# Performance work log

Measured on AMD Instinct MI355X. Metric: run time of the kernel, lower is better.

The kernel has to match this reference:

```python
import jax, jax.numpy as jnp
import numpy as np

TRAN_DIM = 768
N_HEADS = 8
HEAD_DIM = 96
INNER = N_HEADS * HEAD_DIM  # 768


def setup_inputs() -> dict:
    key = jax.random.key(0)
    k1, k2, k3, k4, k5 = jax.random.split(key, 5)
    x = jax.random.normal(k1, (16, 1024, TRAN_DIM), dtype=jnp.float32)
    s_in = 1.0 / np.sqrt(TRAN_DIM)
    W_qkv = jax.random.uniform(k2, (TRAN_DIM, INNER * 3), jnp.float32, -s_in, s_in)
    b_qkv = jax.random.uniform(k3, (INNER * 3,), jnp.float32, -s_in, s_in)
    s_o = 1.0 / np.sqrt(INNER)
    W_out = jax.random.uniform(k4, (INNER, TRAN_DIM), jnp.float32, -s_o, s_o)
    b_out = jax.random.uniform(k5, (TRAN_DIM,), jnp.float32, -s_o, s_o)
    return {"x": x, "W_qkv": W_qkv, "b_qkv": b_qkv, "W_out": W_out, "b_out": b_out}


def reference(x, W_qkv, b_qkv, W_out, b_out):
    B, N, _ = x.shape
    qkv = x @ W_qkv + b_qkv  # [B, N, 3*INNER]
    q, k, v = jnp.split(qkv, 3, axis=-1)
    # [B, N, INNER] -> [B, H, N, D]
    def to_heads(t):
        return t.reshape(B, N, N_HEADS, HEAD_DIM).transpose(0, 2, 1, 3)
    q, k, v = to_heads(q), to_heads(k), to_heads(v)
    scale = HEAD_DIM ** (-0.5)
    dots = jnp.einsum('bhnd,bhmd->bhnm', q, k) * scale
    attn = jax.nn.softmax(dots, axis=-1)
    out = jnp.einsum('bhnm,bhmd->bhnd', attn, v)
    out = out.transpose(0, 2, 1, 3).reshape(B, N, INNER)
    return out @ W_out + b_out
```

## Files before the change

kernel.cpp:

```cpp
#include <hip/hip_runtime.h>
#include <hip/hip_bf16.h>


#define DEVINL __device__ __forceinline__

typedef __attribute__((ext_vector_type(8))) short s16x8;
typedef __attribute__((ext_vector_type(4))) short s16x4;
typedef __attribute__((ext_vector_type(4))) float f32x4;
typedef __attribute__((ext_vector_type(16))) float f32x16;

DEVINL short f2bf(float f) {
  union { float f; unsigned u; } c; c.f = f;
  unsigned r = c.u + 0x7FFFu + ((c.u >> 16) & 1u);
  return (short)(r >> 16);
}
DEVINL float asf(unsigned u) {
  union { unsigned u; float f; } c; c.u = u; return c.f;
}
DEVINL unsigned pack2(float a, float b) {
  union { float f; unsigned u; } ca, cb; ca.f = a; cb.f = b;
  return (ca.u >> 16) | (cb.u & 0xffff0000u);
}
DEVINL int swap23(int k) { return (k & ~12) | ((k & 4) << 1) | ((k & 8) >> 1); }

DEVINL void gload_lds16(const short* g, short* lds) {
  __builtin_amdgcn_global_load_lds((const __attribute__((address_space(1))) void*)g,
                                   (__attribute__((address_space(3))) void*)lds, 16, 0, 0);
}


__global__ void cvt_x_kernel(const float* __restrict__ in, short* __restrict__ out) {
  int i = blockIdx.x * 256 + threadIdx.x;
  float4 v = ((const float4*)in)[i];
  s16x4 o = { f2bf(v.x), f2bf(v.y), f2bf(v.z), f2bf(v.w) };
  *(s16x4*)(out + (size_t)i * 4) = o;
}

__global__ void tcvt_kernel(const float* __restrict__ in, short* __restrict__ out, int R, int C) {
  __shared__ float t[32][33];
  int tx = threadIdx.x & 31, ty = threadIdx.x >> 5;
  int r0 = blockIdx.y * 32, c0 = blockIdx.x * 32;
#pragma unroll
  for (int i = 0; i < 4; i++) {
    int r = ty + i * 8;
    t[r][tx] = in[(size_t)(r0 + r) * C + c0 + tx];
  }
  __syncthreads();
#pragma unroll
  for (int i = 0; i < 4; i++) {
    int r = ty + i * 8;
    out[(size_t)(c0 + r) * R + r0 + tx] = f2bf(t[tx][r]);
  }
}

__global__ void vtrans_kernel(const short* __restrict__ qkvb, short* __restrict__ out) {
  __shared__ short t[32][34];
  int tx = threadIdx.x & 31, ty = threadIdx.x >> 5;
  int d0 = blockIdx.x * 32, n0 = blockIdx.y * 32;
  int pair = blockIdx.z;
  int b = pair >> 3, h = pair & 7;
#pragma unroll
  for (int i = 0; i < 4; i++) {
    int r = ty + i * 8;
    t[r][tx] = qkvb[(size_t)(b * 1024 + n0 + r) * 2304 + 1536 + h * 96 + d0 + tx];
  }
  __syncthreads();
  size_t obase = (size_t)pair * 96 * 1024;
#pragma unroll
  for (int i = 0; i < 4; i++) {
    int r = ty + i * 8;
    out[obase + (size_t)(d0 + r) * 1024 + n0 + tx] = t[tx][r];
  }
}


template <int MODE>
__global__ __launch_bounds__(512, 4) void gemm2(const short* __restrict__ A, const short* __restrict__ Bt,
                                                const float* __restrict__ bias, int K, int nTn,
                                                short* __restrict__ qkvb, float* __restrict__ outf) {
  __shared__ short lds[36864];
  short* const ldsA = lds;
  short* const ldsB = lds + 24576;
  const int tid = threadIdx.x;
  const int l = tid & 63, w = tid >> 6;
  const int lo = l & 15, hi = l >> 4;
  const int wm = w >> 1, wn = w & 1;

  int cpx = gridDim.x >> 3;
  int bid = blockIdx.x;
  int swz = (bid & 7) * cpx + (bid >> 3);
  int tm = swz / nTn, tn = swz - tm * nTn;

  const int NKT = K >> 5;

  const int Ls = tid >> 3, s7 = tid & 7;
  const int pS = (s7 >> 2) & 1;
  const int cS = (s7 & 3) ^ (Ls & 3);
  const int rho = 2 * Ls + pS;
  const int gA = ((rho >> 5) << 6) + (rho & 31);
  const short* aS0 = A + (size_t)(tm * 256 + gA) * K + cS * 8;
  const short* aS1 = aS0 + (size_t)32 * K;
  const short* bS = Bt + (size_t)(tn * 128 + rho) * K + cS * 8;

#define ST_A(j, q, bs) gload_lds16(((q) ? aS1 : aS0) + (j) * 32, ldsA + ((bs) * 2 + (q)) * 4096 + tid * 8)
#define ST_B(j, bs)    gload_lds16(bS + (j) * 32, ldsB + (bs) * 4096 + tid * 8)

  const int LaBase = wm * 16 + (lo >> 1);
  const int LbBase = wn * 32 + (lo >> 1);
  const int pp = (lo & 1) << 2;

  f32x4 acc[4][4] = {};

#define RD_A(AF, bc, qm) do {                                                    \
    const short* base_ = ldsA + ((bc) * 2 + (qm)) * 4096;                        \
    _Pragma("unroll") for (int mi = 0; mi < 2; mi++) {                           \
      int La_ = LaBase + mi * 8;                                                 \
      AF[mi] = *(const s16x8*)(base_ + La_ * 64 + (((hi ^ (La_ & 3)) + pp) << 3)); } } while (0)
#define RD_B(BF, bc) do {                                                        \
    const short* base_ = ldsB + (bc) * 4096;                                     \
    _Pragma("unroll") for (int b = 0; b < 4; b++) {                              \
      int Lb_ = LbBase + b * 8;                                                  \
      BF[b] = *(const s16x8*)(base_ + Lb_ * 64 + (((hi ^ (Lb_ & 3)) + pp) << 3)); } } while (0)

#define MM8(a0, AF, BF) do {                                                     \
    __builtin_amdgcn_s_setprio(1);                                               \
    _Pragma("unroll") for (int mi = 0; mi < 2; mi++)                             \
      _Pragma("unroll") for (int b = 0; b < 4; b++)                              \
        acc[(a0) + mi][b] = __builtin_amdgcn_mfma_f32_16x16x32_bf16(             \
            AF[mi], BF[b], acc[(a0) + mi][b], 0, 0, 0);                          \
    __builtin_amdgcn_s_setprio(0); } while (0)

#define WAITV(n) asm volatile("s_waitcnt vmcnt(" #n ")" ::: "memory")
#define BARR() do { __builtin_amdgcn_sched_barrier(0); __builtin_amdgcn_s_barrier(); \
                    __builtin_amdgcn_sched_barrier(0); } while (0)

  ST_A(0, 0, 0); ST_B(0, 0); ST_A(0, 1, 0);
  ST_A(1, 0, 1); ST_B(1, 1); ST_A(1, 1, 1);
  WAITV(3);
  __builtin_amdgcn_s_barrier();

  s16x8 af[2], bf[4];
  int bc = 0;
#pragma unroll 1
  for (int kt = 0; kt < NKT; kt++) {
    int bs = (bc == 0) ? 2 : bc - 1;
    RD_A(af, bc, 0);
    RD_B(bf, bc);
    if (kt + 2 < NKT) { ST_A(kt + 2, 0, bs); ST_B(kt + 2, bs); }
    MM8(0, af, bf);
    RD_A(af, bc, 1);
    if (kt + 2 < NKT) ST_A(kt + 2, 1, bs);
    MM8(2, af, bf);
    if (kt + 2 < NKT) {
      WAITV(3);
    } else if (kt + 2 == NKT) {
      WAITV(0);
    }
    BARR();
    bc = (bc == 2) ? 0 : bc + 1;
  }
#undef ST_A
#undef ST_B
#undef RD_A
#undef RD_B
#undef MM8
#undef WAITV
#undef BARR

  if (MODE == 0) {
    const float qscale = 0.14724444757204526f;
    __syncthreads();
#pragma unroll
    for (int b = 0; b < 4; b++) {
      int colr = wn * 64 + b * 16 + lo;
      int coln = tn * 128 + colr;
      float bv = bias[coln];
      float scl = (coln < 768) ? qscale : 1.0f;
#pragma unroll
      for (int a = 0; a < 4; a++)
#pragma unroll
        for (int j = 0; j < 4; j++) {
          int rowr = wm * 64 + a * 16 + hi * 4 + j;
          lds[rowr * 128 + colr] = f2bf((acc[a][b][j] + bv) * scl);
        }
    }
    __syncthreads();
    short* dstb = qkvb + (size_t)(tm * 256) * 2304 + tn * 128;
#pragma unroll
    for (int k = 0; k < 8; k++) {
      int g = k * 512 + tid;
      int r = g >> 4, c = g & 15;
      *(s16x8*)(dstb + (size_t)r * 2304 + c * 8) = *(const s16x8*)(lds + r * 128 + c * 8);
    }
  } else {
#pragma unroll
    for (int b = 0; b < 4; b++) {
      int coln = tn * 128 + wn * 64 + b * 16 + lo;
      float bv = bias[coln];
#pragma unroll
      for (int a = 0; a < 4; a++)
#pragma unroll
        for (int j = 0; j < 4; j++) {
          int rowm = tm * 256 + wm * 64 + a * 16 + hi * 4 + j;
          outf[(size_t)rowm * 768 + coln] = acc[a][b][j] + bv;
        }
    }
  }
}


__global__ __launch_bounds__(256) void attn_kernel(const short* __restrict__ qkvb,
                                                   const short* __restrict__ vtb,
                                                   short* __restrict__ attn_out) {
  __shared__ short Klds[64 * 104];
  __shared__ short Vlds[96 * 64];
  int tid = threadIdx.x, lane = tid & 63, wid = tid >> 6;
  int q31 = lane & 31, hi2 = lane >> 5;
  int bid = blockIdx.x;
  int pair = bid & 127, qt = bid >> 7;
  int b = pair >> 3, h = pair & 7;
  const short* Vtp = vtb + (size_t)pair * 1024 * 96;
  int qrow0 = qt * 128 + wid * 32;

  s16x8 qf[6];
#pragma unroll
  for (int dc = 0; dc < 6; dc++)
    qf[dc] = *(const s16x8*)(qkvb + (size_t)(b * 1024 + qrow0 + q31) * 2304 +
                             h * 96 + dc * 16 + hi2 * 8);

  const short* sp[6];
  short* sdst[6];
  int sstep[6];
#pragma unroll
  for (int i = 0; i < 6; i++) {
    if (i < 3) {
      int c = i * 256 + tid;
      int krow = c / 12, kcc = c - krow * 12;
      int lam = swap23(krow);
      sdst[i] = Klds + lam * 104 + kcc * 8;
      sp[i] = qkvb + (size_t)(b * 1024 + krow) * 2304 + 768 + h * 96 + kcc * 8;
      sstep[i] = 64 * 2304;
    } else {
      int d = (i - 3) * 256 + tid;
      int vrow = d >> 3, vcc = d & 7;
      sdst[i] = Vlds + vrow * 64 + ((vcc ^ (vrow & 7)) << 3);
      sp[i] = Vtp + (size_t)vrow * 1024 + vcc * 8;
      sstep[i] = 64;
    }
  }

  f32x16 accO[3] = {};
  float lsum = 0.0f;

  s16x8 sreg[6];
#pragma unroll
  for (int i = 0; i < 6; i++) sreg[i] = *(const s16x8*)sp[i];

  for (int t = 0; t < 16; t++) {
    __syncthreads();
#pragma unroll
    for (int i = 0; i < 6; i++) *(s16x8*)sdst[i] = sreg[i];
    __syncthreads();

    int t2 = (t + 1) & 15;
#pragma unroll
    for (int i = 0; i < 6; i++)
      sreg[i] = *(const s16x8*)(sp[i] + (size_t)t2 * sstep[i]);

#pragma unroll
    for (int kb = 0; kb < 2; kb++) {
      f32x16 st = {};
#pragma unroll
      for (int dc = 0; dc < 6; dc++) {
        int c = dc * 2 + hi2;
        int lam = kb * 32 + q31;
        s16x8 kf = *(const s16x8*)(Klds + lam * 104 + c * 8);
        st = __builtin_amdgcn_mfma_f32_32x32x16_bf16(kf, qf[dc], st, 0, 0, 0);
      }

      unsigned u[8];
#pragma unroll
      for (int i = 0; i < 8; i++) {
        float p0 = __builtin_amdgcn_exp2f(st[2 * i]);
        float p1 = __builtin_amdgcn_exp2f(st[2 * i + 1]);
        unsigned w = pack2(p0, p1);
        u[i] = w;
        lsum += asf(w << 16) + asf(w & 0xffff0000u);
      }

#pragma unroll
      for (int half = 0; half < 2; half++) {
        union { unsigned w[4]; s16x8 v; } pa;
#pragma unroll
        for (int wi = 0; wi < 4; wi++) pa.w[wi] = u[half * 4 + wi];
        int kc = kb * 2 + half;
#pragma unroll
        for (int db = 0; db < 3; db++) {
          int d = db * 32 + q31;
          s16x8 vf = *(const s16x8*)(Vlds + d * 64 + (((kc * 2 + hi2) ^ (d & 7)) << 3));
          accO[db] = __builtin_amdgcn_mfma_f32_32x32x16_bf16(pa.v, vf, accO[db], 0, 0, 0);
        }
      }
    }
  }

  float s = lsum + __shfl_xor(lsum, 32, 64);
  float rinv = 1.0f / s;
  float rr[16];
#pragma unroll
  for (int r = 0; r < 16; r++)
    rr[r] = __shfl(rinv, (r & 3) + 8 * (r >> 2) + 4 * hi2, 64);

#pragma unroll
  for (int db = 0; db < 3; db++)
#pragma unroll
    for (int r = 0; r < 16; r++) {
      int qrow = qrow0 + (r & 3) + 8 * (r >> 2) + 4 * hi2;
      int d = db * 32 + q31;
      attn_out[((size_t)b * 1024 + qrow) * 768 + h * 96 + d] = f2bf(accO[db][r] * rr[r]);
    }
}


extern "C" void kernel_launch(void* const* d_in, const int* in_sizes, int n_in,
                              void* d_out, int out_size, void* d_ws, size_t ws_size,
                              hipStream_t stream) {
  const float* x = (const float*)d_in[0];
  const float* Wqkv = (const float*)d_in[1];
  const float* bqkv = (const float*)d_in[2];
  const float* Wout = (const float*)d_in[3];
  const float* bout = (const float*)d_in[4];
  float* out = (float*)d_out;

  char* ws = (char*)d_ws;
  short* xb = (short*)ws;
  short* wqkvT = (short*)(ws + 25165824);
  short* woutT = (short*)(ws + 28704768);
  short* qkvb = (short*)(ws + 29884416);
  short* vtb = (short*)(ws + 105381888);

  cvt_x_kernel<<<12288, 256, 0, stream>>>(x, xb);
  tcvt_kernel<<<dim3(72, 24), 256, 0, stream>>>(Wqkv, wqkvT, 768, 2304);
  tcvt_kernel<<<dim3(24, 24), 256, 0, stream>>>(Wout, woutT, 768, 768);

  gemm2<0><<<1152, 512, 0, stream>>>(xb, wqkvT, bqkv, 768, 18, qkvb, nullptr);
  vtrans_kernel<<<dim3(3, 32, 128), 256, 0, stream>>>(qkvb, vtb);
  attn_kernel<<<1024, 256, 0, stream>>>(qkvb, vtb, xb);
  gemm2<1><<<384, 512, 0, stream>>>(xb, woutT, bout, 768, 6, nullptr, out);
}
```

Baseline: 188.9 us.

## Fuse V transpose into QKV GEMM epilogue and add MFMA priority hints

Result: faster. 182.8 us (median of 2 runs) (-3.2%).

```diff
diff --git a/kernel.cpp b/kernel.cpp
--- a/kernel.cpp
+++ b/kernel.cpp
@@ -53,31 +53,12 @@
   }
 }
 
-__global__ void vtrans_kernel(const short* __restrict__ qkvb, short* __restrict__ out) {
-  __shared__ short t[32][34];
-  int tx = threadIdx.x & 31, ty = threadIdx.x >> 5;
-  int d0 = blockIdx.x * 32, n0 = blockIdx.y * 32;
-  int pair = blockIdx.z;
-  int b = pair >> 3, h = pair & 7;
-#pragma unroll
-  for (int i = 0; i < 4; i++) {
-    int r = ty + i * 8;
-    t[r][tx] = qkvb[(size_t)(b * 1024 + n0 + r) * 2304 + 1536 + h * 96 + d0 + tx];
-  }
-  __syncthreads();
-  size_t obase = (size_t)pair * 96 * 1024;
-#pragma unroll
-  for (int i = 0; i < 4; i++) {
-    int r = ty + i * 8;
-    out[obase + (size_t)(d0 + r) * 1024 + n0 + tx] = t[tx][r];
-  }
-}
-
 
 template <int MODE>
 __global__ __launch_bounds__(512, 4) void gemm2(const short* __restrict__ A, const short* __restrict__ Bt,
                                                 const float* __restrict__ bias, int K, int nTn,
-                                                short* __restrict__ qkvb, float* __restrict__ outf) {
+                                                short* __restrict__ qkvb, short* __restrict__ vtb,
+                                                float* __restrict__ outf) {
   __shared__ short lds[36864];
   short* const ldsA = lds;
   short* const ldsB = lds + 24576;
@@ -170,27 +151,61 @@
   if (MODE == 0) {
     const float qscale = 0.14724444757204526f;
     __syncthreads();
-#pragma unroll
-    for (int b = 0; b < 4; b++) {
-      int colr = wn * 64 + b * 16 + lo;
-      int coln = tn * 128 + colr;
-      float bv = bias[coln];
-      float scl = (coln < 768) ? qscale : 1.0f;
-#pragma unroll
-      for (int a = 0; a < 4; a++)
-#pragma unroll
-        for (int j = 0; j < 4; j++) {
-          int rowr = wm * 64 + a * 16 + hi * 4 + j;
-          lds[rowr * 128 + colr] = f2bf((acc[a][b][j] + bv) * scl);
-        }
-    }
-    __syncthreads();
-    short* dstb = qkvb + (size_t)(tm * 256) * 2304 + tn * 128;
-#pragma unroll
-    for (int k = 0; k < 8; k++) {
-      int g = k * 512 + tid;
-      int r = g >> 4, c = g & 15;
-      *(s16x8*)(dstb + (size_t)r * 2304 + c * 8) = *(const s16x8*)(lds + r * 128 + c * 8);
+    if (tn < 12) {
+#pragma unroll
+      for (int b = 0; b < 4; b++) {
+        int colr = wn * 64 + b * 16 + lo;
+        int coln = tn * 128 + colr;
+        float bv = bias[coln];
+        float scl = (coln < 768) ? qscale : 1.0f;
+#pragma unroll
+        for (int a = 0; a < 4; a++)
+#pragma unroll
+          for (int j = 0; j < 4; j++) {
+            int rowr = wm * 64 + a * 16 + hi * 4 + j;
+            lds[rowr * 128 + colr] = f2bf((acc[a][b][j] + bv) * scl);
+          }
+      }
+      __syncthreads();
+      short* dstb = qkvb + (size_t)(tm * 256) * 2304 + tn * 128;
+#pragma unroll
+      for (int k = 0; k < 8; k++) {
+        int g = k * 512 + tid;
+        int r = g >> 4, c = g & 15;
+        *(s16x8*)(dstb + (size_t)r * 2304 + c * 8) = *(const s16x8*)(lds + r * 128 + c * 8);
+      }
+    } else {
+      short* scr = lds + w * 4096;
+#pragma unroll
+      for (int b = 0; b < 4; b++) {
+        int c = b * 16 + lo;
+        float bv = bias[tn * 128 + wn * 64 + c];
+#pragma unroll
+        for (int a = 0; a < 4; a++)
+#pragma unroll
+          for (int j = 0; j < 4; j++) {
+            int row = a * 16 + hi * 4 + j;
+            scr[row * 64 + (c ^ (((row >> 3) & 7) << 3))] = f2bf(acc[a][b][j] + bv);
+          }
+      }
+      int r8 = l >> 3;
+      int k8 = l & 7;
+      int n0 = k8 * 8;
+      int rowg = tm * 256 + wm * 64;
+      int bb = rowg >> 10;
+      int nb = (rowg & 1023) + n0;
+#pragma unroll
+      for (int p = 0; p < 8; p++) {
+        int c = p * 8 + r8;
+        int inner = tn * 128 + wn * 64 + c - 1536;
+        int hh = inner / 96;
+        int dd = inner - hh * 96;
+        union { short v[8]; s16x8 x; } t;
+#pragma unroll
+        for (int j = 0; j < 8; j++)
+          t.v[j] = scr[(n0 + j) * 64 + (c ^ (k8 << 3))];
+        *(s16x8*)(vtb + ((size_t)(bb * 8 + hh) * 96 + dd) * 1024 + nb) = t.x;
+      }
     }
   } else {
 #pragma unroll
@@ -270,6 +285,7 @@
 #pragma unroll
     for (int kb = 0; kb < 2; kb++) {
       f32x16 st = {};
+      __builtin_amdgcn_s_setprio(1);
 #pragma unroll
       for (int dc = 0; dc < 6; dc++) {
         int c = dc * 2 + hi2;
@@ -277,6 +293,7 @@
         s16x8 kf = *(const s16x8*)(Klds + lam * 104 + c * 8);
         st = __builtin_amdgcn_mfma_f32_32x32x16_bf16(kf, qf[dc], st, 0, 0, 0);
       }
+      __builtin_amdgcn_s_setprio(0);
 
       unsigned u[8];
 #pragma unroll
@@ -288,6 +305,7 @@
         lsum += asf(w << 16) + asf(w & 0xffff0000u);
       }
 
+      __builtin_amdgcn_s_setprio(1);
 #pragma unroll
       for (int half = 0; half < 2; half++) {
         union { unsigned w[4]; s16x8 v; } pa;
@@ -301,6 +319,7 @@
           accO[db] = __builtin_amdgcn_mfma_f32_32x32x16_bf16(pa.v, vf, accO[db], 0, 0, 0);
         }
       }
+      __builtin_amdgcn_s_setprio(0);
     }
   }
 
@@ -343,8 +362,7 @@
   tcvt_kernel<<<dim3(72, 24), 256, 0, stream>>>(Wqkv, wqkvT, 768, 2304);
   tcvt_kernel<<<dim3(24, 24), 256, 0, stream>>>(Wout, woutT, 768, 768);
 
-  gemm2<0><<<1152, 512, 0, stream>>>(xb, wqkvT, bqkv, 768, 18, qkvb, nullptr);
-  vtrans_kernel<<<dim3(3, 32, 128), 256, 0, stream>>>(qkvb, vtb);
+  gemm2<0><<<1152, 512, 0, stream>>>(xb, wqkvT, bqkv, 768, 18, qkvb, vtb, nullptr);
   attn_kernel<<<1024, 256, 0, stream>>>(qkvb, vtb, xb);
-  gemm2<1><<<384, 512, 0, stream>>>(xb, woutT, bout, 768, 6, nullptr, out);
-}
+  gemm2<1><<<384, 512, 0, stream>>>(xb, woutT, bout, 768, 6, nullptr, nullptr, out);
+}
```
